# Performance work log

Hardware: AMD Instinct MI355X
Metric: run time of the kernel (lower is better)

Reference implementation:

```python
import jax, jax.numpy as jnp
import numpy as np

H = 16        # head_nums
DN = 128      # qk_nope_head_dim
DR = 64       # qk_rope_head_dim
DV = 128      # v_head_dim
QLR = 1536    # q_lora_rank
KVLR = 512    # kv_lora_rank
HID = 2048    # hidden_dim
THETA = 10000.0
EPS = 1e-6


def _rms(x, w):
    return x * jax.lax.rsqrt(jnp.mean(x * x, axis=-1, keepdims=True) + EPS) * w


def _reorder(x):
    # replicates view(b,h,s,d//2,2).transpose(4,3).reshape: [x0,x2,...,x1,x3,...]
    return jnp.concatenate([x[..., 0::2], x[..., 1::2]], axis=-1)


def _rotate_half(x):
    h = x.shape[-1] // 2
    return jnp.concatenate([-x[..., h:], x[..., :h]], axis=-1)


def setup_inputs() -> dict:
    key = jax.random.key(0)
    ks = jax.random.split(key, 7)
    B, S = 1, 2048

    def w(k, i, o):
        return jax.random.normal(k, (i, o), jnp.float32) * (i ** -0.5)

    return {
        "x": jax.random.normal(ks[0], (B, S, HID), jnp.float32),
        "Wq_down": w(ks[1], HID, QLR),
        "q_norm_w": jnp.ones((QLR,), jnp.float32),
        "Wq_up": w(ks[2], QLR, H * (DN + DR)),
        "Wkv_down": w(ks[3], HID, KVLR + DR),
        "kv_norm_w": jnp.ones((KVLR,), jnp.float32),
        "Wkv_up": w(ks[4], KVLR, H * (DN + DV)),
        "Wo": w(ks[5], HID, HID),
        "position": jnp.broadcast_to(jnp.arange(S, dtype=jnp.int32)[None], (B, S)),
        "mask": jnp.tril(jnp.ones((S, S), bool))[None, None],  # causal [1,1,S,S]
    }


def reference(x, Wq_down, q_norm_w, Wq_up, Wkv_down, kv_norm_w, Wkv_up, Wo, position, mask):
    B, S, _ = x.shape
    # low-rank Q path: down-proj -> RMSNorm -> up-proj -> [B,H,S,DN+DR]
    q = _rms(x @ Wq_down, q_norm_w) @ Wq_up
    q = q.reshape(B, S, H, DN + DR).transpose(0, 2, 1, 3)
    q_nope, q_rope = q[..., :DN], q[..., DN:]
    # latent KV path
    ckv = x @ Wkv_down
    c, k_rope = ckv[..., :KVLR], ckv[..., KVLR:]
    c = _rms(c, kv_norm_w)
    kv = (c @ Wkv_up).reshape(B, S, H, DN + DV).transpose(0, 2, 1, 3)
    k_nope, v = kv[..., :DN], kv[..., DN:]
    k_rope = k_rope[:, None]  # [B,1,S,DR] shared across heads
    # rotary tables
    inv_freq = 1.0 / (THETA ** (jnp.arange(0, DR, 2, dtype=jnp.float32) / DR))
    t = jnp.arange(S, dtype=jnp.float32)
    emb = jnp.concatenate([jnp.outer(t, inv_freq)] * 2, axis=-1)  # [S,DR]
    cos = jnp.cos(emb)[position][:, None]  # [B,1,S,DR]
    sin = jnp.sin(emb)[position][:, None]
    qr, kr = _reorder(q_rope), _reorder(k_rope)
    q_rot = qr * cos + _rotate_half(qr) * sin
    k_rot = kr * cos + _rotate_half(kr) * sin
    q_state = jnp.concatenate([q_nope, q_rot], axis=-1)              # [B,H,S,DN+DR]
    k_state = jnp.concatenate(
        [k_nope, jnp.broadcast_to(k_rot, (B, H, S, DR))], axis=-1)   # [B,H,S,DN+DR]
    scores = jnp.einsum('bhsd,bhtd->bhst', q_state, k_state) / np.float32(np.sqrt(DV))
    scores = jnp.where(mask, scores, -jnp.inf)
    att = jax.nn.softmax(scores, axis=-1)
    out = jnp.einsum('bhst,bhtd->bhsd', att, v)
    out = out.transpose(0, 2, 1, 3).reshape(B, S, H * DV)
    return out @ Wo
```

## Files before the change

### kernel.cpp

```cpp
#include <hip/hip_runtime.h>
#include <hip/hip_bf16.h>
#include <cstddef>

#define H 16
#define DN 128
#define DR 64
#define DV 128
#define QLR 1536
#define KVLR 512
#define HID 2048
#define SLEN 2048
#define EPS 1e-6f
#define SCALE 0.08838834764831845f
#define QK_SCALE (0.08838834764831845f * 1.4426950408889634f)

typedef __attribute__((ext_vector_type(8))) short short8;
typedef __attribute__((ext_vector_type(4))) float f32x4;
typedef unsigned short u16;

__device__ __forceinline__ u16 f2bf(float f) {
    __hip_bfloat16 h = __float2bfloat16(f);
    return __builtin_bit_cast(u16, h);
}
__device__ __forceinline__ float b2f(u16 v) {
    return __bfloat162float(__builtin_bit_cast(__hip_bfloat16, v));
}
__device__ __forceinline__ unsigned pack2(float a, float b) {
    return (unsigned)f2bf(a) | ((unsigned)f2bf(b) << 16);
}

__global__ __launch_bounds__(256) void prep_all(
    const float* __restrict__ x, u16* __restrict__ xb,
    const float* __restrict__ Wqd, const float* __restrict__ Wkvd,
    const float* __restrict__ Wqu, const float* __restrict__ Wkvu,
    const float* __restrict__ Wo,
    u16* __restrict__ BtF, u16* __restrict__ Wqu_t,
    u16* __restrict__ Wkvu_t, u16* __restrict__ Wo_t)
{
    const int tid = threadIdx.x;
    if (blockIdx.x < 2048) {
        size_t base = ((size_t)blockIdx.x * 256 + tid) * 8;
        float4 v0 = *reinterpret_cast<const float4*>(x + base);
        float4 v1 = *reinterpret_cast<const float4*>(x + base + 4);
        union { short8 s; unsigned u[4]; } p;
        p.u[0] = pack2(v0.x, v0.y); p.u[1] = pack2(v0.z, v0.w);
        p.u[2] = pack2(v1.x, v1.y); p.u[3] = pack2(v1.z, v1.w);
        *reinterpret_cast<short8*>(xb + base) = p.s;
        return;
    }
    int b = blockIdx.x - 2048;
    const float* W; u16* Wt; int K, N, nx; float scale = 1.0f;
    if (b < 768)       { W = Wqd;  Wt = BtF;                          K = 2048; N = 1536; nx = 24; }
    else if (b < 1088) { b -= 768;  W = Wkvd; Wt = BtF + (size_t)1536 * 2048; K = 2048; N = 576;  nx = 10; }
    else if (b < 2240) { b -= 1088; W = Wqu;  Wt = Wqu_t;             K = 1536; N = 3072; nx = 48; scale = QK_SCALE; }
    else if (b < 2752) { b -= 2240; W = Wkvu; Wt = Wkvu_t;            K = 512;  N = 4096; nx = 64; }
    else               { b -= 2752; W = Wo;   Wt = Wo_t;              K = 2048; N = 2048; nx = 32; }
    const int bx = b % nx, by = b / nx;

    __shared__ float T[64][65];
    const int n0 = bx * 64, k0 = by * 64;
    const bool inb = (n0 < N);
    {
        int r = tid >> 4, c4 = (tid & 15) * 4;
        #pragma unroll
        for (int rr = 0; rr < 4; ++rr) {
            int row = rr * 16 + r;
            float4 v = inb ? *reinterpret_cast<const float4*>(W + (size_t)(k0 + row) * N + n0 + c4)
                           : make_float4(0.f, 0.f, 0.f, 0.f);
            T[row][c4] = v.x * scale; T[row][c4 + 1] = v.y * scale;
            T[row][c4 + 2] = v.z * scale; T[row][c4 + 3] = v.w * scale;
        }
    }
    __syncthreads();
    {
        int n = tid >> 2, kq = (tid & 3) * 16;
        unsigned u[8];
        #pragma unroll
        for (int jj = 0; jj < 8; ++jj)
            u[jj] = pack2(T[kq + 2 * jj][n], T[kq + 2 * jj + 1][n]);
        u16* dst = Wt + (size_t)(n0 + n) * K + k0 + kq;
        *reinterpret_cast<uint4*>(dst)     = make_uint4(u[0], u[1], u[2], u[3]);
        *reinterpret_cast<uint4*>(dst + 8) = make_uint4(u[4], u[5], u[6], u[7]);
    }
}

__device__ __forceinline__ void stage4(const char* Gb, const unsigned* srcOff,
                                       const int* ldsBase, u16* smemBuf, unsigned koff)
{
    #pragma unroll
    for (int j = 0; j < 4; ++j)
        __builtin_amdgcn_global_load_lds(
            (const __attribute__((address_space(1))) unsigned int*)(Gb + srcOff[j] + koff),
            (__attribute__((address_space(3))) unsigned int*)(smemBuf + ldsBase[j]),
            16, 0, 0);
}

template<bool BF16OUT>
__device__ __forceinline__ void gemm_core(
    const u16* __restrict__ A, const u16* __restrict__ Bt, void* __restrict__ Cv,
    int N, int K, int m0, int n0, u16 (*smem)[8192])
{
    const int tid = threadIdx.x, lane = tid & 63, w = tid >> 6;
    const size_t Kb = (size_t)K * 2;

    unsigned srcOff[4];
    int ldsBase[4];
    #pragma unroll
    for (int j = 0; j < 4; ++j) {
        int c = w * 4 + j;
        int o = (c & 7) * 1024 + lane * 16;
        int u = o ^ (((o >> 7) & 3) << 4);
        int row = u >> 6, kbyte = u & 63;
        srcOff[j] = (unsigned)((size_t)((c < 8 ? m0 : n0) + row) * Kb + kbyte);
        ldsBase[j] = (c < 8) ? (c * 512) : (4096 + (c - 8) * 512);
    }
    const char* Gb = (w < 2) ? (const char*)A : (const char*)Bt;

    const int wr = (w >> 1) * 64, wc = (w & 1) * 64;
    int aoff[4], boff[4];
    #pragma unroll
    for (int i = 0; i < 4; ++i) {
        int oa = (wr + i * 16 + (lane & 15)) * 64 + (lane >> 4) * 16;
        aoff[i] = oa ^ (((oa >> 7) & 3) << 4);
        int ob = (wc + i * 16 + (lane & 15)) * 64 + (lane >> 4) * 16;
        boff[i] = (ob ^ (((ob >> 7) & 3) << 4)) + 8192;
    }

    f32x4 acc[4][4];
    #pragma unroll
    for (int i = 0; i < 4; ++i)
        #pragma unroll
        for (int j = 0; j < 4; ++j) acc[i][j] = (f32x4){0.f, 0.f, 0.f, 0.f};

    const int NT = K >> 5;
    stage4(Gb, srcOff, ldsBase, &smem[0][0], 0);
    __syncthreads();
    int cur = 0;
    for (int t = 0; t < NT; ++t) {
        if (t + 1 < NT) stage4(Gb, srcOff, ldsBase, &smem[cur ^ 1][0], (unsigned)(t + 1) * 64);
        const char* base = (const char*)&smem[cur][0];
        short8 af[4], bfr[4];
        #pragma unroll
        for (int i = 0; i < 4; ++i) af[i] = *reinterpret_cast<const short8*>(base + aoff[i]);
        #pragma unroll
        for (int i = 0; i < 4; ++i) bfr[i] = *reinterpret_cast<const short8*>(base + boff[i]);
        __builtin_amdgcn_s_setprio(1);
        #pragma unroll
        for (int i = 0; i < 4; ++i)
            #pragma unroll
            for (int j = 0; j < 4; ++j)
                acc[i][j] = __builtin_amdgcn_mfma_f32_16x16x32_bf16(af[i], bfr[j], acc[i][j], 0, 0, 0);
        __builtin_amdgcn_s_setprio(0);
        __syncthreads();
        cur ^= 1;
    }

    #pragma unroll
    for (int i = 0; i < 4; ++i) {
        int grow0 = m0 + wr + i * 16 + ((lane >> 4) * 4);
        #pragma unroll
        for (int j = 0; j < 4; ++j) {
            int gcol = n0 + wc + j * 16 + (lane & 15);
            if (gcol < N) {
                #pragma unroll
                for (int r = 0; r < 4; ++r) {
                    float v2 = acc[i][j][r];
                    if (BF16OUT) ((u16*)Cv)[(size_t)(grow0 + r) * N + gcol] = f2bf(v2);
                    else         ((float*)Cv)[(size_t)(grow0 + r) * N + gcol] = v2;
                }
            }
        }
    }
}

template<bool BF16OUT>
__global__ __launch_bounds__(256) void gemm_bf16(
    const u16* __restrict__ A, const u16* __restrict__ Bt,
    void* __restrict__ Cv, int M, int N, int K)
{
    __shared__ u16 smem[2][8192];
    const int nbx = gridDim.x, nby = gridDim.y;
    const int nwg = nbx * nby;
    int orig = blockIdx.y * nbx + blockIdx.x;
    int xcd = orig & 7, o8 = orig >> 3;
    int qq = nwg >> 3, rr = nwg & 7;
    int v = (xcd < rr ? xcd * (qq + 1) : rr * (qq + 1) + (xcd - rr) * qq) + o8;
    int bx = v / nby, by = v - bx * nby;
    gemm_core<BF16OUT>(A, Bt, Cv, N, K, by * 128, bx * 128, smem);
}

__global__ __launch_bounds__(256) void gemm_dual(
    const u16* __restrict__ Aq, const u16* __restrict__ Bq, u16* __restrict__ Cq,
    const u16* __restrict__ Ak, const u16* __restrict__ Bk, u16* __restrict__ Ck)
{
    __shared__ u16 smem[2][8192];
    int b = blockIdx.x;
    const u16 *A, *Bt; u16* C; int N, K, nbx;
    if (b < 384) { A = Aq; Bt = Bq; C = Cq; N = 3072; K = 1536; nbx = 24; }
    else { b -= 384; A = Ak; Bt = Bk; C = Ck; N = 4096; K = 512; nbx = 32; }
    const int nwg = nbx * 16;
    int xcd = b & 7, o8 = b >> 3;
    int qq = nwg >> 3, rr = nwg & 7;
    int v = (xcd < rr ? xcd * (qq + 1) : rr * (qq + 1) + (xcd - rr) * qq) + o8;
    int bx = v / 16, by = v - bx * 16;
    gemm_core<true>(A, Bt, C, N, K, by * 128, bx * 128, smem);
}

__global__ __launch_bounds__(256) void rmsnorm2_bf16(
    const float* __restrict__ fC, const float* __restrict__ qw,
    const float* __restrict__ kvw, u16* __restrict__ qdb, u16* __restrict__ ckvb)
{
    const int row = blockIdx.x, tid = threadIdx.x;
    const float* p = fC + (size_t)row * 2112;
    float ssq = 0.f, ssk = 0.f;
    for (int i = tid * 4; i < 1536; i += 1024) {
        float4 v = *reinterpret_cast<const float4*>(p + i);
        ssq += v.x * v.x + v.y * v.y + v.z * v.z + v.w * v.w;
    }
    if (tid < 128) {
        float4 v = *reinterpret_cast<const float4*>(p + 1536 + tid * 4);
        ssk = v.x * v.x + v.y * v.y + v.z * v.z + v.w * v.w;
    }
    __shared__ float wsq[4], wsk[4];
    int lane = tid & 63, wv = tid >> 6;
    #pragma unroll
    for (int off = 32; off; off >>= 1) {
        ssq += __shfl_down(ssq, off);
        ssk += __shfl_down(ssk, off);
    }
    if (lane == 0) { wsq[wv] = ssq; wsk[wv] = ssk; }
    __syncthreads();
    if (tid == 0) {
        wsq[0] = rsqrtf((wsq[0] + wsq[1] + wsq[2] + wsq[3]) / 1536.f + EPS);
        wsk[0] = rsqrtf((wsk[0] + wsk[1] + wsk[2] + wsk[3]) / 512.f + EPS);
    }
    __syncthreads();
    float scq = wsq[0], sck = wsk[0];
    for (int i = tid * 4; i < 1536; i += 1024) {
        float4 v = *reinterpret_cast<const float4*>(p + i);
        float4 g = *reinterpret_cast<const float4*>(qw + i);
        *reinterpret_cast<uint2*>(qdb + (size_t)row * 1536 + i) =
            make_uint2(pack2(v.x * scq * g.x, v.y * scq * g.y),
                       pack2(v.z * scq * g.z, v.w * scq * g.w));
    }
    if (tid < 128) {
        int i = tid * 4;
        float4 v = *reinterpret_cast<const float4*>(p + 1536 + i);
        float4 g = *reinterpret_cast<const float4*>(kvw + i);
        *reinterpret_cast<uint2*>(ckvb + (size_t)row * 512 + i) =
            make_uint2(pack2(v.x * sck * g.x, v.y * sck * g.y),
                       pack2(v.z * sck * g.z, v.w * sck * g.w));
    }
}

__global__ __launch_bounds__(256) void rope_bf16(
    u16* __restrict__ q, const float* __restrict__ krsrc, int krStride,
    u16* __restrict__ krot)
{
    const int s = blockIdx.x, tid = threadIdx.x;
    __shared__ float cs[32], sn[32];
    if (tid < 32) {
        float inv = powf(10000.0f, -(float)tid / 32.0f);
        float ang = (float)s * inv;
        cs[tid] = cosf(ang); sn[tid] = sinf(ang);
    }
    __syncthreads();
    float ev[2], ov[2]; int hh[2], ii[2];
    #pragma unroll
    for (int it = 0; it < 2; ++it) {
        int pidx = tid + it * 256;
        int h = pidx >> 5, i = pidx & 31;
        hh[it] = h; ii[it] = i;
        const u16* base = q + (size_t)s * 3072 + h * 192 + 128;
        ev[it] = b2f(base[2 * i]); ov[it] = b2f(base[2 * i + 1]);
    }
    __syncthreads();
    #pragma unroll
    for (int it = 0; it < 2; ++it) {
        int h = hh[it], i = ii[it];
        u16* base = q + (size_t)s * 3072 + h * 192 + 128;
        base[i]      = f2bf(ev[it] * cs[i] - ov[it] * sn[i]);
        base[32 + i] = f2bf(ov[it] * cs[i] + ev[it] * sn[i]);
    }
    if (tid < 32) {
        int i = tid;
        float e = krsrc[(size_t)s * krStride + 2 * i];
        float o = krsrc[(size_t)s * krStride + 2 * i + 1];
        krot[(size_t)s * 64 + i]      = f2bf(e * cs[i] - o * sn[i]);
        krot[(size_t)s * 64 + 32 + i] = f2bf(o * cs[i] + e * sn[i]);
    }
}

__global__ __launch_bounds__(256) void vtrans(
    const u16* __restrict__ kvbf, u16* __restrict__ vtb)
{
    const int bid = blockIdx.x;
    const int h = bid & 15, rem = bid >> 4;
    const int st = rem & 31, dt = rem >> 5;
    __shared__ u16 T[64][72];
    const int tid = threadIdx.x;
    #pragma unroll
    for (int it = 0; it < 2; ++it) {
        int c = it * 256 + tid;
        int r = c >> 3, c8 = (c & 7) * 8;
        short8 v = *reinterpret_cast<const short8*>(
            kvbf + ((size_t)(st * 64 + r) * 16 + h) * 256 + 128 + dt * 64 + c8);
        *reinterpret_cast<short8*>(&T[r][c8]) = v;
    }
    __syncthreads();
    #pragma unroll
    for (int it = 0; it < 2; ++it) {
        int c = it * 256 + tid;
        int d = c >> 3, s8 = (c & 7) * 8;
        union { short8 s; u16 e[8]; } o;
        #pragma unroll
        for (int j = 0; j < 8; ++j) o.e[j] = T[s8 + j][d];
        *reinterpret_cast<short8*>(
            vtb + ((size_t)(h * 128 + dt * 64 + d)) * 2048 + st * 64 + s8) = o.s;
    }
}

__global__ __launch_bounds__(256, 2) void attn_chunk(
    const u16* __restrict__ qbf,
    const u16* __restrict__ kvbf,
    const u16* __restrict__ krot,
    const u16* __restrict__ vtb,
    u16* __restrict__ outb,
    u16* __restrict__ partAcc,
    float* __restrict__ partML)
{
    const int bid = blockIdx.x;
    const int xcd = bid & 7, slot = bid >> 3;
    const int h = xcd + 8 * (slot & 1);
    const int r80 = 79 - (slot >> 1);
    int qb, ch, S, poff;
    if (r80 < 8)       { qb = r80;                 ch = 0;      S = 1; poff = 0; }
    else if (r80 < 24) { int u = r80 - 8;  qb = 8 + (u >> 1);  ch = u & 1; S = 2; poff = (qb - 8) * 2 + ch; }
    else if (r80 < 48) { int u = r80 - 24; qb = 16 + u / 3;    ch = u % 3; S = 3; poff = 16 + (qb - 16) * 3 + ch; }
    else               { int u = r80 - 48; qb = 24 + (u >> 2); ch = u & 3; S = 4; poff = 40 + (qb - 24) * 4 + ch; }
    const int s0 = qb * 64;
    const int t0 = ch * 8;
    const int t1 = (t0 + 8 < qb + 1) ? (t0 + 8) : (qb + 1);
    const int slotId = h * 72 + poff;
    const int tid = threadIdx.x, lane = tid & 63, w = tid >> 6;
    const int colk = lane & 15, grp = lane >> 4, g8 = grp * 8;

    __shared__ u16 Ks[64 * 192];
    __shared__ u16 Vt[128 * 64];

    const int qg = s0 + w * 16 + colk;

    short8 qreg[6];
    {
        const u16* qp = qbf + ((size_t)qg * H + h) * 192;
        #pragma unroll
        for (int ks = 0; ks < 6; ++ks)
            qreg[ks] = *reinterpret_cast<const short8*>(qp + ks * 32 + g8);
    }

    int kt[6], kslot[6];
    #pragma unroll
    for (int it = 0; it < 6; ++it) {
        int c = it * 256 + tid;
        kt[it] = c / 24; kslot[it] = c % 24;
    }
    int vr[4], vks_[4];
    #pragma unroll
    for (int it = 0; it < 4; ++it) {
        int c = it * 256 + tid;
        vr[it] = c >> 3; vks_[it] = c & 7;
    }

    short8 kreg[6], vregV[4];

    auto issue_loads = [&](int t) {
        #pragma unroll
        for (int it = 0; it < 6; ++it) {
            int gk = t * 64 + kt[it];
            const u16* src = (kslot[it] < 16)
                ? kvbf + ((size_t)gk * H + h) * 256 + kslot[it] * 8
                : krot + (size_t)gk * 64 + (kslot[it] - 16) * 8;
            kreg[it] = *reinterpret_cast<const short8*>(src);
        }
// ... 152 lines not shown
__global__ __launch_bounds__(256) void attn_combine(
    const u16* __restrict__ partAcc, const float* __restrict__ partML,
    u16* __restrict__ outb)
{
    const int bid = blockIdx.x;
    const int xcd = bid & 7, s2 = bid >> 3;
    const int h = xcd + 8 * (s2 / 24);
    const int qb = 8 + s2 % 24;
    int S, poff;
    if (qb < 16)      { S = 2; poff = (qb - 8) * 2; }
    else if (qb < 24) { S = 3; poff = 16 + (qb - 16) * 3; }
    else              { S = 4; poff = 40 + (qb - 24) * 4; }
    const int base = h * 72 + poff;
    const int tid = threadIdx.x;
    const int row = tid >> 2, seg = (tid & 3) * 32;

    float mv[4], lv[4];
    float m_g = -1e30f;
    #pragma unroll
    for (int s = 0; s < 4; ++s) {
        bool ok = (s < S);
        mv[s] = ok ? partML[(size_t)(base + s) * 128 + row * 2]     : -1e30f;
        lv[s] = ok ? partML[(size_t)(base + s) * 128 + row * 2 + 1] : 0.f;
        m_g = fmaxf(m_g, mv[s]);
    }
    float l_g = 0.f, wq[4];
    #pragma unroll
    for (int s = 0; s < 4; ++s) { wq[s] = exp2f(mv[s] - m_g); l_g += wq[s] * lv[s]; }
    float inv = 1.f / l_g;
    u16* orow = outb + (size_t)(qb * 64 + row) * 2048 + h * 128 + seg;
    #pragma unroll
    for (int i = 0; i < 8; ++i) {
        float o[4] = {0.f, 0.f, 0.f, 0.f};
        #pragma unroll
        for (int s = 0; s < 4; ++s) {
            if (s < S) {
                ushort4 a = *reinterpret_cast<const ushort4*>(
                    partAcc + (size_t)(base + s) * 8192 + row * 128 + seg + i * 4);
                o[0] += wq[s] * b2f(a.x); o[1] += wq[s] * b2f(a.y);
                o[2] += wq[s] * b2f(a.z); o[3] += wq[s] * b2f(a.w);
            }
        }
        uint2 pk;
        pk.x = pack2(o[0] * inv, o[1] * inv);
        pk.y = pack2(o[2] * inv, o[3] * inv);
        *reinterpret_cast<uint2*>(orow + i * 4) = pk;
    }
}

extern "C" void kernel_launch(void* const* d_in, const int* in_sizes, int n_in,
                              void* d_out, int out_size, void* d_ws, size_t ws_size,
                              hipStream_t stream)
{
    (void)in_sizes; (void)n_in; (void)out_size; (void)ws_size;
    const float* x         = (const float*)d_in[0];
    const float* Wq_down   = (const float*)d_in[1];
    const float* q_norm_w  = (const float*)d_in[2];
    const float* Wq_up     = (const float*)d_in[3];
    const float* Wkv_down  = (const float*)d_in[4];
    const float* kv_norm_w = (const float*)d_in[5];
    const float* Wkv_up    = (const float*)d_in[6];
    const float* Wo        = (const float*)d_in[7];
    float* out = (float*)d_out;

    char* p = (char*)d_ws;
    u16* BtF     = (u16*)p;   p += (size_t)2176 * 2048 * 2;
    u16* Wkvu_t  = (u16*)p;   p += (size_t)4096 * 512  * 2;
    u16* Wo_t    = (u16*)p;   p += (size_t)2048 * 2048 * 2;
    u16* qbuf    = (u16*)p;   p += (size_t)2048 * 3072 * 2;
    u16* ckvb    = (u16*)p;   p += (size_t)2048 * 512  * 2;
    u16* kvbf    = (u16*)p;   p += (size_t)2048 * 4096 * 2;
    u16* krotb   = (u16*)p;   p += (size_t)2048 * 64   * 2;
    char* pool   = p;
    u16* xb      = (u16*)p;   p += (size_t)2048 * 2048 * 2;
    u16* Wqu_t   = (u16*)p;   p += (size_t)3072 * 1536 * 2;
    float* fC    = (float*)p; p += (size_t)2048 * 2112 * 4;
    u16* qdb     = (u16*)p;   p += (size_t)2048 * 1536 * 2;
    u16* attb    = (u16*)BtF;
    u16* partAcc = xb;
    float* partML  = (float*)(partAcc + (size_t)1152 * 8192);
    u16* vtb     = (u16*)(pool + (size_t)20 * 1024 * 1024);

    dim3 blk(256);
    prep_all<<<5824, blk, 0, stream>>>(x, xb, Wq_down, Wkv_down, Wq_up, Wkv_up, Wo,
                                       BtF, Wqu_t, Wkvu_t, Wo_t);

    gemm_bf16<false><<<dim3(17, 16), blk, 0, stream>>>(xb, BtF, fC, 2048, 2112, 2048);
    rmsnorm2_bf16<<<2048, blk, 0, stream>>>(fC, q_norm_w, kv_norm_w, qdb, ckvb);
    gemm_dual<<<dim3(896), blk, 0, stream>>>(qdb, Wqu_t, qbuf, ckvb, Wkvu_t, kvbf);
    rope_bf16<<<2048, blk, 0, stream>>>(qbuf, fC + 2048, 2112, krotb);
    vtrans<<<dim3(1024), blk, 0, stream>>>(kvbf, vtb);

    attn_chunk<<<dim3(1280), blk, 0, stream>>>(qbuf, kvbf, krotb, vtb, attb, partAcc, partML);
    attn_combine<<<dim3(384), blk, 0, stream>>>(partAcc, partML, attb);

    gemm_bf16<false><<<dim3(16, 16), blk, 0, stream>>>(attb, Wo_t, out, 2048, 2048, 2048);
}
```

Before: 208.3 us.

## Overlap weight casts with down-proj GEMM, fuse rope/vtrans, use BK64 GEMM

Moves the up-projection and output weight transpose-casts out of the prep kernel and into the down-projection GEMM launch as extra blocks, so that memory-bound conversion overlaps with the matrix-multiply work. Merges the rope and V-transpose kernels into one launch to save a launch boundary. Adds a GEMM core with a 64-wide K tile, double-buffered at 64 KB of LDS, for the down-projection and Wo GEMMs. The larger LDS footprint may reduce occupancy, and co-scheduling the cast blocks can compete with the GEMM for bandwidth.

```diff
diff --git a/kernel.cpp b/kernel.cpp
--- a/kernel.cpp
+++ b/kernel.cpp
@@ -29,13 +29,42 @@
     return (unsigned)f2bf(a) | ((unsigned)f2bf(b) << 16);
 }
 
+__device__ __forceinline__ void tcast_block(
+    const float* __restrict__ W, u16* __restrict__ Wt,
+    int K, int N, int nx, float scale, int b, float (*T)[65])
+{
+    const int tid = threadIdx.x;
+    const int bx = b % nx, by = b / nx;
+    const int n0 = bx * 64, k0 = by * 64;
+    const bool inb = (n0 < N);
+    {
+        int r = tid >> 4, c4 = (tid & 15) * 4;
+        #pragma unroll
+        for (int rr = 0; rr < 4; ++rr) {
+            int row = rr * 16 + r;
+            float4 v = inb ? *reinterpret_cast<const float4*>(W + (size_t)(k0 + row) * N + n0 + c4)
+                           : make_float4(0.f, 0.f, 0.f, 0.f);
+            T[row][c4] = v.x * scale; T[row][c4 + 1] = v.y * scale;
+            T[row][c4 + 2] = v.z * scale; T[row][c4 + 3] = v.w * scale;
+        }
+    }
+    __syncthreads();
+    {
+        int n = tid >> 2, kq = (tid & 3) * 16;
+        unsigned u[8];
+        #pragma unroll
+        for (int jj = 0; jj < 8; ++jj)
+            u[jj] = pack2(T[kq + 2 * jj][n], T[kq + 2 * jj + 1][n]);
+        u16* dst = Wt + (size_t)(n0 + n) * K + k0 + kq;
+        *reinterpret_cast<uint4*>(dst)     = make_uint4(u[0], u[1], u[2], u[3]);
+        *reinterpret_cast<uint4*>(dst + 8) = make_uint4(u[4], u[5], u[6], u[7]);
+    }
+}
+
 __global__ __launch_bounds__(256) void prep_all(
     const float* __restrict__ x, u16* __restrict__ xb,
     const float* __restrict__ Wqd, const float* __restrict__ Wkvd,
-    const float* __restrict__ Wqu, const float* __restrict__ Wkvu,
-    const float* __restrict__ Wo,
-    u16* __restrict__ BtF, u16* __restrict__ Wqu_t,
-    u16* __restrict__ Wkvu_t, u16* __restrict__ Wo_t)
+    u16* __restrict__ BtF)
 {
     const int tid = threadIdx.x;
     if (blockIdx.x < 2048) {
@@ -48,40 +77,10 @@
         *reinterpret_cast<short8*>(xb + base) = p.s;
         return;
     }
+    __shared__ float T[64][65];
     int b = blockIdx.x - 2048;
-    const float* W; u16* Wt; int K, N, nx; float scale = 1.0f;
-    if (b < 768)       { W = Wqd;  Wt = BtF;                          K = 2048; N = 1536; nx = 24; }
-    else if (b < 1088) { b -= 768;  W = Wkvd; Wt = BtF + (size_t)1536 * 2048; K = 2048; N = 576;  nx = 10; }
-    else if (b < 2240) { b -= 1088; W = Wqu;  Wt = Wqu_t;             K = 1536; N = 3072; nx = 48; scale = QK_SCALE; }
-    else if (b < 2752) { b -= 2240; W = Wkvu; Wt = Wkvu_t;            K = 512;  N = 4096; nx = 64; }
-    else               { b -= 2752; W = Wo;   Wt = Wo_t;              K = 2048; N = 2048; nx = 32; }
-    const int bx = b % nx, by = b / nx;
-
-    __shared__ float T[64][65];
-    const int n0 = bx * 64, k0 = by * 64;
-    const bool inb = (n0 < N);
-    {
-        int r = tid >> 4, c4 = (tid & 15) * 4;
-        #pragma unroll
-        for (int rr = 0; rr < 4; ++rr) {
-            int row = rr * 16 + r;
-            float4 v = inb ? *reinterpret_cast<const float4*>(W + (size_t)(k0 + row) * N + n0 + c4)
-                           : make_float4(0.f, 0.f, 0.f, 0.f);
-            T[row][c4] = v.x * scale; T[row][c4 + 1] = v.y * scale;
-            T[row][c4 + 2] = v.z * scale; T[row][c4 + 3] = v.w * scale;
-        }
-    }
-    __syncthreads();
-    {
-        int n = tid >> 2, kq = (tid & 3) * 16;
-        unsigned u[8];
-        #pragma unroll
-        for (int jj = 0; jj < 8; ++jj)
-            u[jj] = pack2(T[kq + 2 * jj][n], T[kq + 2 * jj + 1][n]);
-        u16* dst = Wt + (size_t)(n0 + n) * K + k0 + kq;
-        *reinterpret_cast<uint4*>(dst)     = make_uint4(u[0], u[1], u[2], u[3]);
-        *reinterpret_cast<uint4*>(dst + 8) = make_uint4(u[4], u[5], u[6], u[7]);
-    }
+    if (b < 768) tcast_block(Wqd, BtF, 2048, 1536, 24, 1.0f, b, T);
+    else         tcast_block(Wkvd, BtF + (size_t)1536 * 2048, 2048, 576, 10, 1.0f, b - 768, T);
 }
 
 __device__ __forceinline__ void stage4(const char* Gb, const unsigned* srcOff,
@@ -171,22 +170,6 @@
             }
         }
     }
-}
-
-template<bool BF16OUT>
-__global__ __launch_bounds__(256) void gemm_bf16(
-    const u16* __restrict__ A, const u16* __restrict__ Bt,
-    void* __restrict__ Cv, int M, int N, int K)
-{
-    __shared__ u16 smem[2][8192];
-    const int nbx = gridDim.x, nby = gridDim.y;
-    const int nwg = nbx * nby;
-    int orig = blockIdx.y * nbx + blockIdx.x;
-    int xcd = orig & 7, o8 = orig >> 3;
-    int qq = nwg >> 3, rr = nwg & 7;
-    int v = (xcd < rr ? xcd * (qq + 1) : rr * (qq + 1) + (xcd - rr) * qq) + o8;
-    int bx = v / nby, by = v - bx * nby;
-    gemm_core<BF16OUT>(A, Bt, Cv, N, K, by * 128, bx * 128, smem);
 }
 
 __global__ __launch_bounds__(256) void gemm_dual(
@@ -206,6 +189,139 @@
     gemm_core<true>(A, Bt, C, N, K, by * 128, bx * 128, smem);
 }
 
+__device__ __forceinline__ void stage8(const char* Gb, const unsigned* srcOff,
+                                       const int* ldsBase, u16* smemBuf, unsigned koff)
+{
+    #pragma unroll
+    for (int j = 0; j < 8; ++j)
+        __builtin_amdgcn_global_load_lds(
+            (const __attribute__((address_space(1))) unsigned int*)(Gb + srcOff[j] + koff),
+            (__attribute__((address_space(3))) unsigned int*)(smemBuf + ldsBase[j]),
+            16, 0, 0);
+}
+
+template<bool BF16OUT>
+__device__ __forceinline__ void gemm_core64(
+    const u16* __restrict__ A, const u16* __restrict__ Bt, void* __restrict__ Cv,
+    int N, int K, int m0, int n0, u16 (*smem)[16384])
+{
+    const int tid = threadIdx.x, lane = tid & 63, w = tid >> 6;
+    const size_t Kb = (size_t)K * 2;
+
+    unsigned srcOff[8];
+    int ldsBase[8];
+    #pragma unroll
+    for (int j = 0; j < 8; ++j) {
+        int c = w * 8 + j;
+        int cc = c & 15;
+        int o = cc * 1024 + lane * 16;
+        int u = o ^ (((o >> 7) & 7) << 4);
+        int row = u >> 7, kbyte = u & 127;
+        srcOff[j] = (unsigned)((size_t)((c < 16 ? m0 : n0) + row) * Kb + kbyte);
+        ldsBase[j] = (c < 16) ? (cc * 512) : (8192 + cc * 512);
+    }
+    const char* Gb = (w < 2) ? (const char*)A : (const char*)Bt;
+
+    const int wr = (w >> 1) * 64, wc = (w & 1) * 64;
+    int aoff[8], boff[8];
+    #pragma unroll
+    for (int ks = 0; ks < 2; ++ks)
+        #pragma unroll
+        for (int i = 0; i < 4; ++i) {
+            int rowa = wr + i * 16 + (lane & 15);
+            int oa = rowa * 128 + ks * 64 + (lane >> 4) * 16;
+            aoff[ks * 4 + i] = oa ^ ((rowa & 7) << 4);
+            int rowb = wc + i * 16 + (lane & 15);
+            int ob = rowb * 128 + ks * 64 + (lane >> 4) * 16;
+            boff[ks * 4 + i] = (ob ^ ((rowb & 7) << 4)) + 16384;
+        }
+
+    f32x4 acc[4][4];
+    #pragma unroll
+    for (int i = 0; i < 4; ++i)
+        #pragma unroll
+        for (int j = 0; j < 4; ++j) acc[i][j] = (f32x4){0.f, 0.f, 0.f, 0.f};
+
+    const int NT = K >> 6;
+    stage8(Gb, srcOff, ldsBase, &smem[0][0], 0);
+    __syncthreads();
+    int cur = 0;
+    for (int t = 0; t < NT; ++t) {
+        if (t + 1 < NT) stage8(Gb, srcOff, ldsBase, &smem[cur ^ 1][0], (unsigned)(t + 1) * 128);
+        const char* base = (const char*)&smem[cur][0];
+        #pragma unroll
+        for (int ks = 0; ks < 2; ++ks) {
+            short8 af[4], bfr[4];
+            #pragma unroll
+            for (int i = 0; i < 4; ++i) af[i] = *reinterpret_cast<const short8*>(base + aoff[ks * 4 + i]);
+            #pragma unroll
+            for (int i = 0; i < 4; ++i) bfr[i] = *reinterpret_cast<const short8*>(base + boff[ks * 4 + i]);
+            __builtin_amdgcn_s_setprio(1);
+            #pragma unroll
+            for (int i = 0; i < 4; ++i)
+                #pragma unroll
+                for (int j = 0; j < 4; ++j)
+                    acc[i][j] = __builtin_amdgcn_mfma_f32_16x16x32_bf16(af[i], bfr[j], acc[i][j], 0, 0, 0);
+            __builtin_amdgcn_s_setprio(0);
+        }
+        __syncthreads();
+        cur ^= 1;
+    }
+
+    #pragma unroll
+    for (int i = 0; i < 4; ++i) {
+        int grow0 = m0 + wr + i * 16 + ((lane >> 4) * 4);
+        #pragma unroll
+        for (int j = 0; j < 4; ++j) {
+            int gcol = n0 + wc + j * 16 + (lane & 15);
+            if (gcol < N) {
+                #pragma unroll
+                for (int r = 0; r < 4; ++r) {
+                    float v2 = acc[i][j][r];
+                    if (BF16OUT) ((u16*)Cv)[(size_t)(grow0 + r) * N + gcol] = f2bf(v2);
+                    else         ((float*)Cv)[(size_t)(grow0 + r) * N + gcol] = v2;
+                }
+            }
+        }
+    }
+}
+
+__global__ __launch_bounds__(256) void gemm_down_fused(
+    const u16* __restrict__ xb, const u16* __restrict__ BtF, float* __restrict__ fC,
+    const float* __restrict__ Wqu, const float* __restrict__ Wkvu, const float* __restrict__ Wo,
+    u16* __restrict__ Wqu_t, u16* __restrict__ Wkvu_t, u16* __restrict__ Wo_t)
+{
+    __shared__ u16 smem[2][16384];
+    if (blockIdx.x < 272) {
+        const int nwg = 272;
+        int orig = blockIdx.x;
+        int xcd = orig & 7, o8 = orig >> 3;
+        int qq = nwg >> 3, rr = nwg & 7;
+        int v = (xcd < rr ? xcd * (qq + 1) : rr * (qq + 1) + (xcd - rr) * qq) + o8;
+        int bx = v / 16, by = v - bx * 16;
+        gemm_core64<false>(xb, BtF, fC, 2112, 2048, by * 128, bx * 128, smem);
+        return;
+    }
+    float (*T)[65] = reinterpret_cast<float(*)[65]>(&smem[0][0]);
+    int b = blockIdx.x - 272;
+    if (b < 1152)      tcast_block(Wqu,  Wqu_t,  1536, 3072, 48, QK_SCALE, b, T);
+    else if (b < 1664) tcast_block(Wkvu, Wkvu_t, 512,  4096, 64, 1.0f, b - 1152, T);
+    else               tcast_block(Wo,   Wo_t,   2048, 2048, 32, 1.0f, b - 1664, T);
+}
+
+__global__ __launch_bounds__(256) void gemm_wo(
+    const u16* __restrict__ A, const u16* __restrict__ Bt, float* __restrict__ C)
+{
+    __shared__ u16 smem[2][16384];
+    const int nwg = 256;
+    int orig = blockIdx.y * 16 + blockIdx.x;
+    int xcd = orig & 7, o8 = orig >> 3;
+    int qq = nwg >> 3;
+    int v = xcd * qq + o8;
+    int bx = v / 16, by = v - bx * 16;
+    gemm_core64<false>(A, Bt, C, 2048, 2048, by * 128, bx * 128, smem);
+}
+
 __global__ __launch_bounds__(256) void rmsnorm2_bf16(
     const float* __restrict__ fC, const float* __restrict__ qw,
     const float* __restrict__ kvw, u16* __restrict__ qdb, u16* __restrict__ ckvb)
@@ -253,52 +369,50 @@
     }
 }
 
-__global__ __launch_bounds__(256) void rope_bf16(
+__global__ __launch_bounds__(256) void rope_vtrans(
     u16* __restrict__ q, const float* __restrict__ krsrc, int krStride,
-    u16* __restrict__ krot)
-{
-    const int s = blockIdx.x, tid = threadIdx.x;
-    __shared__ float cs[32], sn[32];
-    if (tid < 32) {
-        float inv = powf(10000.0f, -(float)tid / 32.0f);
-        float ang = (float)s * inv;
-        cs[tid] = cosf(ang); sn[tid] = sinf(ang);
-    }
-    __syncthreads();
-    float ev[2], ov[2]; int hh[2], ii[2];
-    #pragma unroll
-    for (int it = 0; it < 2; ++it) {
-        int pidx = tid + it * 256;
-        int h = pidx >> 5, i = pidx & 31;
-        hh[it] = h; ii[it] = i;
-        const u16* base = q + (size_t)s * 3072 + h * 192 + 128;
-        ev[it] = b2f(base[2 * i]); ov[it] = b2f(base[2 * i + 1]);
-    }
-    __syncthreads();
-    #pragma unroll
-    for (int it = 0; it < 2; ++it) {
-        int h = hh[it], i = ii[it];
-        u16* base = q + (size_t)s * 3072 + h * 192 + 128;
-        base[i]      = f2bf(ev[it] * cs[i] - ov[it] * sn[i]);
-        base[32 + i] = f2bf(ov[it] * cs[i] + ev[it] * sn[i]);
-    }
-    if (tid < 32) {
-        int i = tid;
-        float e = krsrc[(size_t)s * krStride + 2 * i];
-        float o = krsrc[(size_t)s * krStride + 2 * i + 1];
-        krot[(size_t)s * 64 + i]      = f2bf(e * cs[i] - o * sn[i]);
-        krot[(size_t)s * 64 + 32 + i] = f2bf(o * cs[i] + e * sn[i]);
-    }
-}
-
-__global__ __launch_bounds__(256) void vtrans(
-    const u16* __restrict__ kvbf, u16* __restrict__ vtb)
-{
-    const int bid = blockIdx.x;
+    u16* __restrict__ krot, const u16* __restrict__ kvbf, u16* __restrict__ vtb)
+{
+    const int tid = threadIdx.x;
+    if (blockIdx.x < 2048) {
+        const int s = blockIdx.x;
+        __shared__ float cs[32], sn[32];
+        if (tid < 32) {
+            float inv = powf(10000.0f, -(float)tid / 32.0f);
+            float ang = (float)s * inv;
+            cs[tid] = cosf(ang); sn[tid] = sinf(ang);
+        }
+        __syncthreads();
+        float ev[2], ov[2]; int hh[2], ii[2];
+        #pragma unroll
+        for (int it = 0; it < 2; ++it) {
+            int pidx = tid + it * 256;
+            int h = pidx >> 5, i = pidx & 31;
+            hh[it] = h; ii[it] = i;
+            const u16* base = q + (size_t)s * 3072 + h * 192 + 128;
+            ev[it] = b2f(base[2 * i]); ov[it] = b2f(base[2 * i + 1]);
+        }
+        __syncthreads();
+        #pragma unroll
+        for (int it = 0; it < 2; ++it) {
+            int h = hh[it], i = ii[it];
+            u16* base = q + (size_t)s * 3072 + h * 192 + 128;
+            base[i]      = f2bf(ev[it] * cs[i] - ov[it] * sn[i]);
+            base[32 + i] = f2bf(ov[it] * cs[i] + ev[it] * sn[i]);
+        }
+        if (tid < 32) {
+            int i = tid;
+            float e = krsrc[(size_t)s * krStride + 2 * i];
+            float o = krsrc[(size_t)s * krStride + 2 * i + 1];
+            krot[(size_t)s * 64 + i]      = f2bf(e * cs[i] - o * sn[i]);
+            krot[(size_t)s * 64 + 32 + i] = f2bf(o * cs[i] + e * sn[i]);
+        }
+        return;
+    }
+    const int bid = blockIdx.x - 2048;
     const int h = bid & 15, rem = bid >> 4;
     const int st = rem & 31, dt = rem >> 5;
     __shared__ u16 T[64][72];
-    const int tid = threadIdx.x;
     #pragma unroll
     for (int it = 0; it < 2; ++it) {
         int c = it * 256 + tid;
@@ -617,17 +731,16 @@
     u16* vtb     = (u16*)(pool + (size_t)20 * 1024 * 1024);
 
     dim3 blk(256);
-    prep_all<<<5824, blk, 0, stream>>>(x, xb, Wq_down, Wkv_down, Wq_up, Wkv_up, Wo,
-                                       BtF, Wqu_t, Wkvu_t, Wo_t);
-
-    gemm_bf16<false><<<dim3(17, 16), blk, 0, stream>>>(xb, BtF, fC, 2048, 2112, 2048);
+    prep_all<<<3136, blk, 0, stream>>>(x, xb, Wq_down, Wkv_down, BtF);
+
+    gemm_down_fused<<<2960, blk, 0, stream>>>(xb, BtF, fC, Wq_up, Wkv_up, Wo,
+                                              Wqu_t, Wkvu_t, Wo_t);
     rmsnorm2_bf16<<<2048, blk, 0, stream>>>(fC, q_norm_w, kv_norm_w, qdb, ckvb);
     gemm_dual<<<dim3(896), blk, 0, stream>>>(qdb, Wqu_t, qbuf, ckvb, Wkvu_t, kvbf);
-    rope_bf16<<<2048, blk, 0, stream>>>(qbuf, fC + 2048, 2112, krotb);
-    vtrans<<<dim3(1024), blk, 0, stream>>>(kvbf, vtb);
+    rope_vtrans<<<3072, blk, 0, stream>>>(qbuf, fC + 2048, 2112, krotb, kvbf, vtb);
 
     attn_chunk<<<dim3(1280), blk, 0, stream>>>(qbuf, kvbf, krotb, vtb, attb, partAcc, partML);
     attn_combine<<<dim3(384), blk, 0, stream>>>(partAcc, partML, attb);
 
-    gemm_bf16<false><<<dim3(16, 16), blk, 0, stream>>>(attb, Wo_t, out, 2048, 2048, 2048);
-}
+    gemm_wo<<<dim3(16, 16), blk, 0, stream>>>(attb, Wo_t, out);
+}
```

After: 190.8 us. 8.4% less time.

## Switch GEMMs to 64x128 tiles with BK=64 and overlap weight casts with GEMM

Applied to the files above, without the earlier changes.

Replaces the 128x128, BK=32 GEMM core with a 64x128 tile and BK=64 core, using wider swizzled LDS staging, so each GEMM launches twice as many workgroups and fills the GPU better. The casts of the up-projection and Wo weights move out of the prep kernel and into the down-projection GEMM launch as extra blocks, so they run alongside it. RoPE and the V transpose are merged into one launch. Smaller tiles reduce operand reuse per block and raise LDS use per block, and fusing heterogeneous blocks can leave the work unevenly balanced.

```diff
diff --git a/kernel.cpp b/kernel.cpp
--- a/kernel.cpp
+++ b/kernel.cpp
@@ -29,13 +29,42 @@
     return (unsigned)f2bf(a) | ((unsigned)f2bf(b) << 16);
 }
 
+__device__ __forceinline__ void tcast_block(
+    const float* __restrict__ W, u16* __restrict__ Wt,
+    int K, int N, int nx, float scale, int b, float (*T)[65])
+{
+    const int tid = threadIdx.x;
+    const int bx = b % nx, by = b / nx;
+    const int n0 = bx * 64, k0 = by * 64;
+    const bool inb = (n0 < N);
+    {
+        int r = tid >> 4, c4 = (tid & 15) * 4;
+        #pragma unroll
+        for (int rr = 0; rr < 4; ++rr) {
+            int row = rr * 16 + r;
+            float4 v = inb ? *reinterpret_cast<const float4*>(W + (size_t)(k0 + row) * N + n0 + c4)
+                           : make_float4(0.f, 0.f, 0.f, 0.f);
+            T[row][c4] = v.x * scale; T[row][c4 + 1] = v.y * scale;
+            T[row][c4 + 2] = v.z * scale; T[row][c4 + 3] = v.w * scale;
+        }
+    }
+    __syncthreads();
+    {
+        int n = tid >> 2, kq = (tid & 3) * 16;
+        unsigned u[8];
+        #pragma unroll
+        for (int jj = 0; jj < 8; ++jj)
+            u[jj] = pack2(T[kq + 2 * jj][n], T[kq + 2 * jj + 1][n]);
+        u16* dst = Wt + (size_t)(n0 + n) * K + k0 + kq;
+        *reinterpret_cast<uint4*>(dst)     = make_uint4(u[0], u[1], u[2], u[3]);
+        *reinterpret_cast<uint4*>(dst + 8) = make_uint4(u[4], u[5], u[6], u[7]);
+    }
+}
+
 __global__ __launch_bounds__(256) void prep_all(
     const float* __restrict__ x, u16* __restrict__ xb,
     const float* __restrict__ Wqd, const float* __restrict__ Wkvd,
-    const float* __restrict__ Wqu, const float* __restrict__ Wkvu,
-    const float* __restrict__ Wo,
-    u16* __restrict__ BtF, u16* __restrict__ Wqu_t,
-    u16* __restrict__ Wkvu_t, u16* __restrict__ Wo_t)
+    u16* __restrict__ BtF)
 {
     const int tid = threadIdx.x;
     if (blockIdx.x < 2048) {
@@ -48,123 +77,108 @@
         *reinterpret_cast<short8*>(xb + base) = p.s;
         return;
     }
+    __shared__ float T[64][65];
     int b = blockIdx.x - 2048;
-    const float* W; u16* Wt; int K, N, nx; float scale = 1.0f;
-    if (b < 768)       { W = Wqd;  Wt = BtF;                          K = 2048; N = 1536; nx = 24; }
-    else if (b < 1088) { b -= 768;  W = Wkvd; Wt = BtF + (size_t)1536 * 2048; K = 2048; N = 576;  nx = 10; }
-    else if (b < 2240) { b -= 1088; W = Wqu;  Wt = Wqu_t;             K = 1536; N = 3072; nx = 48; scale = QK_SCALE; }
-    else if (b < 2752) { b -= 2240; W = Wkvu; Wt = Wkvu_t;            K = 512;  N = 4096; nx = 64; }
-    else               { b -= 2752; W = Wo;   Wt = Wo_t;              K = 2048; N = 2048; nx = 32; }
-    const int bx = b % nx, by = b / nx;
-
-    __shared__ float T[64][65];
-    const int n0 = bx * 64, k0 = by * 64;
-    const bool inb = (n0 < N);
-    {
-        int r = tid >> 4, c4 = (tid & 15) * 4;
-        #pragma unroll
-        for (int rr = 0; rr < 4; ++rr) {
-            int row = rr * 16 + r;
-            float4 v = inb ? *reinterpret_cast<const float4*>(W + (size_t)(k0 + row) * N + n0 + c4)
-                           : make_float4(0.f, 0.f, 0.f, 0.f);
-            T[row][c4] = v.x * scale; T[row][c4 + 1] = v.y * scale;
-            T[row][c4 + 2] = v.z * scale; T[row][c4 + 3] = v.w * scale;
-        }
-    }
-    __syncthreads();
-    {
-        int n = tid >> 2, kq = (tid & 3) * 16;
-        unsigned u[8];
-        #pragma unroll
-        for (int jj = 0; jj < 8; ++jj)
-            u[jj] = pack2(T[kq + 2 * jj][n], T[kq + 2 * jj + 1][n]);
-        u16* dst = Wt + (size_t)(n0 + n) * K + k0 + kq;
-        *reinterpret_cast<uint4*>(dst)     = make_uint4(u[0], u[1], u[2], u[3]);
-        *reinterpret_cast<uint4*>(dst + 8) = make_uint4(u[4], u[5], u[6], u[7]);
-    }
-}
-
-__device__ __forceinline__ void stage4(const char* Gb, const unsigned* srcOff,
+    if (b < 768) tcast_block(Wqd, BtF, 2048, 1536, 24, 1.0f, b, T);
+    else         tcast_block(Wkvd, BtF + (size_t)1536 * 2048, 2048, 576, 10, 1.0f, b - 768, T);
+}
+
+__device__ __forceinline__ void stage6(const char* const* gb, const unsigned* srcOff,
                                        const int* ldsBase, u16* smemBuf, unsigned koff)
 {
     #pragma unroll
-    for (int j = 0; j < 4; ++j)
+    for (int j = 0; j < 6; ++j)
         __builtin_amdgcn_global_load_lds(
-            (const __attribute__((address_space(1))) unsigned int*)(Gb + srcOff[j] + koff),
+            (const __attribute__((address_space(1))) unsigned int*)(gb[j] + srcOff[j] + koff),
             (__attribute__((address_space(3))) unsigned int*)(smemBuf + ldsBase[j]),
             16, 0, 0);
 }
 
 template<bool BF16OUT>
-__device__ __forceinline__ void gemm_core(
+__device__ __forceinline__ void gemm_core64(
     const u16* __restrict__ A, const u16* __restrict__ Bt, void* __restrict__ Cv,
-    int N, int K, int m0, int n0, u16 (*smem)[8192])
+    int N, int K, int m0, int n0, u16 (*smem)[12288])
 {
     const int tid = threadIdx.x, lane = tid & 63, w = tid >> 6;
+    const int colk = lane & 15, grp16 = (lane >> 4) * 16;
     const size_t Kb = (size_t)K * 2;
 
-    unsigned srcOff[4];
-    int ldsBase[4];
-    #pragma unroll
-    for (int j = 0; j < 4; ++j) {
-        int c = w * 4 + j;
-        int o = (c & 7) * 1024 + lane * 16;
-        int u = o ^ (((o >> 7) & 3) << 4);
-        int row = u >> 6, kbyte = u & 63;
-        srcOff[j] = (unsigned)((size_t)((c < 8 ? m0 : n0) + row) * Kb + kbyte);
-        ldsBase[j] = (c < 8) ? (c * 512) : (4096 + (c - 8) * 512);
-    }
-    const char* Gb = (w < 2) ? (const char*)A : (const char*)Bt;
-
-    const int wr = (w >> 1) * 64, wc = (w & 1) * 64;
-    int aoff[4], boff[4];
-    #pragma unroll
-    for (int i = 0; i < 4; ++i) {
-        int oa = (wr + i * 16 + (lane & 15)) * 64 + (lane >> 4) * 16;
-        aoff[i] = oa ^ (((oa >> 7) & 3) << 4);
-        int ob = (wc + i * 16 + (lane & 15)) * 64 + (lane >> 4) * 16;
-        boff[i] = (ob ^ (((ob >> 7) & 3) << 4)) + 8192;
-    }
-
-    f32x4 acc[4][4];
+    const char* gb[6];
+    unsigned srcOff[6];
+    int ldsBase[6];
+    #pragma unroll
+    for (int j = 0; j < 6; ++j) {
+        int c = w * 6 + j;
+        bool isA = (c < 8);
+        int cc = isA ? c : c - 8;
+        int o = cc * 1024 + lane * 16;
+        int u = o ^ (((o >> 7) & 7) << 4);
+        int row = u >> 7, kbyte = u & 127;
+        gb[j] = isA ? (const char*)A : (const char*)Bt;
+        srcOff[j] = (unsigned)((size_t)(isA ? m0 + row : n0 + row) * Kb + kbyte);
+        ldsBase[j] = isA ? cc * 512 : 4096 + cc * 512;
+    }
+
+    const int wc = w * 32;
+    int aoff[8], boff[4];
+    #pragma unroll
+    for (int ks = 0; ks < 2; ++ks) {
+        #pragma unroll
+        for (int i = 0; i < 4; ++i) {
+            int ra = i * 16 + colk;
+            int oa = ra * 128 + ks * 64 + grp16;
+            aoff[ks * 4 + i] = oa ^ ((ra & 7) << 4);
+        }
+        #pragma unroll
+        for (int jj = 0; jj < 2; ++jj) {
+            int rb = wc + jj * 16 + colk;
+            int ob = rb * 128 + ks * 64 + grp16;
+            boff[ks * 2 + jj] = (ob ^ ((rb & 7) << 4)) + 8192;
+        }
+    }
+
+    f32x4 acc[4][2];
     #pragma unroll
     for (int i = 0; i < 4; ++i)
         #pragma unroll
-        for (int j = 0; j < 4; ++j) acc[i][j] = (f32x4){0.f, 0.f, 0.f, 0.f};
-
-    const int NT = K >> 5;
-    stage4(Gb, srcOff, ldsBase, &smem[0][0], 0);
+        for (int j = 0; j < 2; ++j) acc[i][j] = (f32x4){0.f, 0.f, 0.f, 0.f};
+
+    const int NT = K >> 6;
+    stage6(gb, srcOff, ldsBase, &smem[0][0], 0);
     __syncthreads();
     int cur = 0;
     for (int t = 0; t < NT; ++t) {
-        if (t + 1 < NT) stage4(Gb, srcOff, ldsBase, &smem[cur ^ 1][0], (unsigned)(t + 1) * 64);
+        if (t + 1 < NT) stage6(gb, srcOff, ldsBase, &smem[cur ^ 1][0], (unsigned)(t + 1) * 128);
         const char* base = (const char*)&smem[cur][0];
-        short8 af[4], bfr[4];
-        #pragma unroll
-        for (int i = 0; i < 4; ++i) af[i] = *reinterpret_cast<const short8*>(base + aoff[i]);
-        #pragma unroll
-        for (int i = 0; i < 4; ++i) bfr[i] = *reinterpret_cast<const short8*>(base + boff[i]);
-        __builtin_amdgcn_s_setprio(1);
-        #pragma unroll
-        for (int i = 0; i < 4; ++i)
+        #pragma unroll
+        for (int ks = 0; ks < 2; ++ks) {
+            short8 af[4], bfr[2];
             #pragma unroll
-            for (int j = 0; j < 4; ++j)
-                acc[i][j] = __builtin_amdgcn_mfma_f32_16x16x32_bf16(af[i], bfr[j], acc[i][j], 0, 0, 0);
-        __builtin_amdgcn_s_setprio(0);
+            for (int i = 0; i < 4; ++i) af[i] = *reinterpret_cast<const short8*>(base + aoff[ks * 4 + i]);
+            #pragma unroll
+            for (int jj = 0; jj < 2; ++jj) bfr[jj] = *reinterpret_cast<const short8*>(base + boff[ks * 2 + jj]);
+            __builtin_amdgcn_s_setprio(1);
+            #pragma unroll
+            for (int i = 0; i < 4; ++i)
+                #pragma unroll
+                for (int jj = 0; jj < 2; ++jj)
+                    acc[i][jj] = __builtin_amdgcn_mfma_f32_16x16x32_bf16(af[i], bfr[jj], acc[i][jj], 0, 0, 0);
+            __builtin_amdgcn_s_setprio(0);
+        }
         __syncthreads();
         cur ^= 1;
     }
 
     #pragma unroll
     for (int i = 0; i < 4; ++i) {
-        int grow0 = m0 + wr + i * 16 + ((lane >> 4) * 4);
-        #pragma unroll
-        for (int j = 0; j < 4; ++j) {
-            int gcol = n0 + wc + j * 16 + (lane & 15);
+        int grow0 = m0 + i * 16 + (grp16 >> 2);
+        #pragma unroll
+        for (int jj = 0; jj < 2; ++jj) {
+            int gcol = n0 + wc + jj * 16 + colk;
             if (gcol < N) {
                 #pragma unroll
                 for (int r = 0; r < 4; ++r) {
-                    float v2 = acc[i][j][r];
+                    float v2 = acc[i][jj][r];
                     if (BF16OUT) ((u16*)Cv)[(size_t)(grow0 + r) * N + gcol] = f2bf(v2);
                     else         ((float*)Cv)[(size_t)(grow0 + r) * N + gcol] = v2;
                 }
@@ -173,37 +187,54 @@
     }
 }
 
-template<bool BF16OUT>
-__global__ __launch_bounds__(256) void gemm_bf16(
-    const u16* __restrict__ A, const u16* __restrict__ Bt,
-    void* __restrict__ Cv, int M, int N, int K)
-{
-    __shared__ u16 smem[2][8192];
-    const int nbx = gridDim.x, nby = gridDim.y;
-    const int nwg = nbx * nby;
-    int orig = blockIdx.y * nbx + blockIdx.x;
+__device__ __forceinline__ void xcd_map(int orig, int nwg, int nby, int& bx, int& by)
+{
     int xcd = orig & 7, o8 = orig >> 3;
     int qq = nwg >> 3, rr = nwg & 7;
     int v = (xcd < rr ? xcd * (qq + 1) : rr * (qq + 1) + (xcd - rr) * qq) + o8;
-    int bx = v / nby, by = v - bx * nby;
-    gemm_core<BF16OUT>(A, Bt, Cv, N, K, by * 128, bx * 128, smem);
+    bx = v / nby; by = v - bx * nby;
+}
+
+__global__ __launch_bounds__(256) void gemm_down_fused(
+    const u16* __restrict__ xb, const u16* __restrict__ BtF, float* __restrict__ fC,
+    const float* __restrict__ Wqu, const float* __restrict__ Wkvu, const float* __restrict__ Wo,
+    u16* __restrict__ Wqu_t, u16* __restrict__ Wkvu_t, u16* __restrict__ Wo_t)
+{
+    __shared__ u16 smem[2][12288];
+    if (blockIdx.x < 544) {
+        int bx, by;
+        xcd_map(blockIdx.x, 544, 32, bx, by);
+        gemm_core64<false>(xb, BtF, fC, 2112, 2048, by * 64, bx * 128, smem);
+        return;
+    }
+    float (*T)[65] = reinterpret_cast<float(*)[65]>(&smem[0][0]);
+    int b = blockIdx.x - 544;
+    if (b < 1152)      tcast_block(Wqu,  Wqu_t,  1536, 3072, 48, QK_SCALE, b, T);
+    else if (b < 1664) tcast_block(Wkvu, Wkvu_t, 512,  4096, 64, 1.0f, b - 1152, T);
+    else               tcast_block(Wo,   Wo_t,   2048, 2048, 32, 1.0f, b - 1664, T);
 }
 
 __global__ __launch_bounds__(256) void gemm_dual(
     const u16* __restrict__ Aq, const u16* __restrict__ Bq, u16* __restrict__ Cq,
     const u16* __restrict__ Ak, const u16* __restrict__ Bk, u16* __restrict__ Ck)
 {
-    __shared__ u16 smem[2][8192];
+    __shared__ u16 smem[2][12288];
     int b = blockIdx.x;
-    const u16 *A, *Bt; u16* C; int N, K, nbx;
-    if (b < 384) { A = Aq; Bt = Bq; C = Cq; N = 3072; K = 1536; nbx = 24; }
-    else { b -= 384; A = Ak; Bt = Bk; C = Ck; N = 4096; K = 512; nbx = 32; }
-    const int nwg = nbx * 16;
-    int xcd = b & 7, o8 = b >> 3;
-    int qq = nwg >> 3, rr = nwg & 7;
-    int v = (xcd < rr ? xcd * (qq + 1) : rr * (qq + 1) + (xcd - rr) * qq) + o8;
-    int bx = v / 16, by = v - bx * 16;
-    gemm_core<true>(A, Bt, C, N, K, by * 128, bx * 128, smem);
+    const u16 *A, *Bt; u16* C; int N, K, nwg;
+    if (b < 768) { A = Aq; Bt = Bq; C = Cq; N = 3072; K = 1536; nwg = 768; }
+    else { b -= 768; A = Ak; Bt = Bk; C = Ck; N = 4096; K = 512; nwg = 1024; }
+    int bx, by;
+    xcd_map(b, nwg, 32, bx, by);
+    gemm_core64<true>(A, Bt, C, N, K, by * 64, bx * 128, smem);
+}
+
+__global__ __launch_bounds__(256) void gemm_wo(
+    const u16* __restrict__ A, const u16* __restrict__ Bt, float* __restrict__ C)
+{
+    __shared__ u16 smem[2][12288];
+    int bx, by;
+    xcd_map(blockIdx.x, 512, 32, bx, by);
+    gemm_core64<false>(A, Bt, C, 2048, 2048, by * 64, bx * 128, smem);
 }
 
 __global__ __launch_bounds__(256) void rmsnorm2_bf16(
@@ -253,52 +284,50 @@
     }
 }
 
-__global__ __launch_bounds__(256) void rope_bf16(
+__global__ __launch_bounds__(256) void rope_vtrans(
     u16* __restrict__ q, const float* __restrict__ krsrc, int krStride,
-    u16* __restrict__ krot)
-{
-    const int s = blockIdx.x, tid = threadIdx.x;
-    __shared__ float cs[32], sn[32];
-    if (tid < 32) {
-        float inv = powf(10000.0f, -(float)tid / 32.0f);
-        float ang = (float)s * inv;
-        cs[tid] = cosf(ang); sn[tid] = sinf(ang);
-    }
-    __syncthreads();
-    float ev[2], ov[2]; int hh[2], ii[2];
-    #pragma unroll
-    for (int it = 0; it < 2; ++it) {
-        int pidx = tid + it * 256;
-        int h = pidx >> 5, i = pidx & 31;
-        hh[it] = h; ii[it] = i;
-        const u16* base = q + (size_t)s * 3072 + h * 192 + 128;
-        ev[it] = b2f(base[2 * i]); ov[it] = b2f(base[2 * i + 1]);
-    }
-    __syncthreads();
-    #pragma unroll
-    for (int it = 0; it < 2; ++it) {
-        int h = hh[it], i = ii[it];
-        u16* base = q + (size_t)s * 3072 + h * 192 + 128;
-        base[i]      = f2bf(ev[it] * cs[i] - ov[it] * sn[i]);
-        base[32 + i] = f2bf(ov[it] * cs[i] + ev[it] * sn[i]);
-    }
-    if (tid < 32) {
-        int i = tid;
-        float e = krsrc[(size_t)s * krStride + 2 * i];
-        float o = krsrc[(size_t)s * krStride + 2 * i + 1];
-        krot[(size_t)s * 64 + i]      = f2bf(e * cs[i] - o * sn[i]);
-        krot[(size_t)s * 64 + 32 + i] = f2bf(o * cs[i] + e * sn[i]);
-    }
-}
-
-__global__ __launch_bounds__(256) void vtrans(
-    const u16* __restrict__ kvbf, u16* __restrict__ vtb)
-{
-    const int bid = blockIdx.x;
+    u16* __restrict__ krot, const u16* __restrict__ kvbf, u16* __restrict__ vtb)
+{
+    const int tid = threadIdx.x;
+    if (blockIdx.x < 2048) {
+        const int s = blockIdx.x;
+        __shared__ float cs[32], sn[32];
+        if (tid < 32) {
+            float inv = powf(10000.0f, -(float)tid / 32.0f);
+            float ang = (float)s * inv;
+            cs[tid] = cosf(ang); sn[tid] = sinf(ang);
+        }
+        __syncthreads();
+        float ev[2], ov[2]; int hh[2], ii[2];
+        #pragma unroll
+        for (int it = 0; it < 2; ++it) {
+            int pidx = tid + it * 256;
+            int h = pidx >> 5, i = pidx & 31;
+            hh[it] = h; ii[it] = i;
+            const u16* base = q + (size_t)s * 3072 + h * 192 + 128;
+            ev[it] = b2f(base[2 * i]); ov[it] = b2f(base[2 * i + 1]);
+        }
+        __syncthreads();
+        #pragma unroll
+        for (int it = 0; it < 2; ++it) {
+            int h = hh[it], i = ii[it];
+            u16* base = q + (size_t)s * 3072 + h * 192 + 128;
+            base[i]      = f2bf(ev[it] * cs[i] - ov[it] * sn[i]);
+            base[32 + i] = f2bf(ov[it] * cs[i] + ev[it] * sn[i]);
+        }
+        if (tid < 32) {
+            int i = tid;
+            float e = krsrc[(size_t)s * krStride + 2 * i];
+            float o = krsrc[(size_t)s * krStride + 2 * i + 1];
+            krot[(size_t)s * 64 + i]      = f2bf(e * cs[i] - o * sn[i]);
+            krot[(size_t)s * 64 + 32 + i] = f2bf(o * cs[i] + e * sn[i]);
+        }
+        return;
+    }
+    const int bid = blockIdx.x - 2048;
     const int h = bid & 15, rem = bid >> 4;
     const int st = rem & 31, dt = rem >> 5;
     __shared__ u16 T[64][72];
-    const int tid = threadIdx.x;
     #pragma unroll
     for (int it = 0; it < 2; ++it) {
         int c = it * 256 + tid;
@@ -617,17 +646,16 @@
     u16* vtb     = (u16*)(pool + (size_t)20 * 1024 * 1024);
 
     dim3 blk(256);
-    prep_all<<<5824, blk, 0, stream>>>(x, xb, Wq_down, Wkv_down, Wq_up, Wkv_up, Wo,
-                                       BtF, Wqu_t, Wkvu_t, Wo_t);
-
-    gemm_bf16<false><<<dim3(17, 16), blk, 0, stream>>>(xb, BtF, fC, 2048, 2112, 2048);
+    prep_all<<<3136, blk, 0, stream>>>(x, xb, Wq_down, Wkv_down, BtF);
+
+    gemm_down_fused<<<3232, blk, 0, stream>>>(xb, BtF, fC, Wq_up, Wkv_up, Wo,
+                                              Wqu_t, Wkvu_t, Wo_t);
     rmsnorm2_bf16<<<2048, blk, 0, stream>>>(fC, q_norm_w, kv_norm_w, qdb, ckvb);
-    gemm_dual<<<dim3(896), blk, 0, stream>>>(qdb, Wqu_t, qbuf, ckvb, Wkvu_t, kvbf);
-    rope_bf16<<<2048, blk, 0, stream>>>(qbuf, fC + 2048, 2112, krotb);
-    vtrans<<<dim3(1024), blk, 0, stream>>>(kvbf, vtb);
+    gemm_dual<<<dim3(1792), blk, 0, stream>>>(qdb, Wqu_t, qbuf, ckvb, Wkvu_t, kvbf);
+    rope_vtrans<<<3072, blk, 0, stream>>>(qbuf, fC + 2048, 2112, krotb, kvbf, vtb);
 
     attn_chunk<<<dim3(1280), blk, 0, stream>>>(qbuf, kvbf, krotb, vtb, attb, partAcc, partML);
     attn_combine<<<dim3(384), blk, 0, stream>>>(partAcc, partML, attb);
 
-    gemm_bf16<false><<<dim3(16, 16), blk, 0, stream>>>(attb, Wo_t, out, 2048, 2048, 2048);
-}
+    gemm_wo<<<dim3(512), blk, 0, stream>>>(attb, Wo_t, out);
+}
```

After: 187.7 us. -9.9%, faster.
